# Optimization experiments

Measured on AMD Instinct MI355X. Metric: run time of the kernel, lower is better.

Reference implementation:

```python
import jax, jax.numpy as jnp
import numpy as np

N, E, KS, DIM = 6890, 41340, 5, 2
K = KS * KS  # 25 spline kernel buckets


def spline_conv(x, edge_index, pseudo, weight, root, bias):
    """Degree-1 open B-spline conv (SplineGCN), mean aggregation + root + bias.
    x: [N, Fin], weight: [K, Fin, Fout], root: [Fin, Fout], bias: [Fout]."""
    row, col = edge_index[0], edge_index[1]  # target, source
    pos = pseudo * (KS - 1)                   # [E, 2] in [0, KS-1]
    i0 = jnp.clip(jnp.floor(pos), 0, KS - 2).astype(jnp.int32)  # [E, 2]
    frac = pos - i0                           # [E, 2]
    # 4 nonzero basis products per edge (2 per dim)
    off = jnp.array([[0, 0], [1, 0], [0, 1], [1, 1]], dtype=jnp.int32)  # [4, 2]
    b_dim = jnp.stack([1.0 - frac, frac], axis=-1)  # [E, 2, 2] (dim, which-knot)
    w = b_dim[:, 0, off[:, 0]] * b_dim[:, 1, off[:, 1]]       # [E, 4]
    idx = (i0[:, None, 0] + off[None, :, 0]) + KS * (i0[:, None, 1] + off[None, :, 1])  # [E, 4]
    # transform all nodes by all K kernels once: [N, K, Fout]
    xw = jnp.einsum('ni,kio->nko', x, weight)
    g = xw[col[:, None], idx]                 # [E, 4, Fout] gather
    msg = jnp.einsum('es,eso->eo', w, g)      # [E, Fout]
    agg = jax.ops.segment_sum(msg, row, num_segments=N)
    deg = jax.ops.segment_sum(jnp.ones((E,), x.dtype), row, num_segments=N)
    agg = agg / jnp.maximum(deg, 1.0)[:, None]
    return agg + x @ root + bias


def setup_inputs() -> dict:
    key = jax.random.key(0)
    ks = jax.random.split(key, 20)
    def gl(k, shape):  # glorot-ish
        fan = shape[-2] if len(shape) > 1 else shape[-1]
        return jax.random.normal(k, shape, jnp.float32) / np.sqrt(fan)
    inp = {
        'x': jax.random.normal(ks[0], (N, 544), jnp.float32),
        'edge_index': jax.random.randint(ks[1], (2, E), 0, N),
        'pseudo': jax.random.uniform(ks[2], (E, DIM), jnp.float32),
        'W_lin': gl(ks[3], (544, 16)), 'b_lin': jnp.zeros((16,), jnp.float32),
        'w1': gl(ks[4], (K, 16, 32)),  'r1': gl(ks[5], (16, 32)),  'bi1': jnp.zeros((32,), jnp.float32),
        'w2': gl(ks[6], (K, 32, 64)),  'r2': gl(ks[7], (32, 64)),  'bi2': jnp.zeros((64,), jnp.float32),
        'w3': gl(ks[8], (K, 64, 128)), 'r3': gl(ks[9], (64, 128)), 'bi3': jnp.zeros((128,), jnp.float32),
        'W1': gl(ks[10], (128, 256)), 'b1': jnp.zeros((256,), jnp.float32),
        'W2': gl(ks[11], (256, 6890)), 'b2': jnp.zeros((6890,), jnp.float32),
    }
    return inp


def reference(x, edge_index, pseudo, W_lin, b_lin, w1, r1, bi1, w2, r2, bi2, w3, r3, bi3, W1, b1, W2, b2):
    h = jax.nn.elu(x @ W_lin + b_lin)
    h = jax.nn.elu(spline_conv(h, edge_index, pseudo, w1, r1, bi1))
    h = jax.nn.elu(spline_conv(h, edge_index, pseudo, w2, r2, bi2))
    h = jax.nn.elu(spline_conv(h, edge_index, pseudo, w3, r3, bi3))
    h = jax.nn.elu(h @ W1 + b1)
    # dropout is identity in eval mode
    logits = h @ W2 + b2
    return jax.nn.log_softmax(logits, axis=-1)
```

## Files before the change

kernel.cpp:

```cpp
#include <hip/hip_runtime.h>
#include <hip/hip_bf16.h>

#define NND 6890
#define NED 41340

typedef __bf16 bf16x8 __attribute__((ext_vector_type(8)));
typedef float f32x4 __attribute__((ext_vector_type(4)));
typedef unsigned short u16x4 __attribute__((ext_vector_type(4)));

__device__ inline unsigned short f32_bf16(float f) {
  unsigned int u = __float_as_uint(f);
  unsigned int r = (u + 0x7FFFu + ((u >> 16) & 1u)) >> 16;
  return (unsigned short)r;
}
__device__ inline void split2(float v, unsigned short& hi, unsigned short& lo) {
  unsigned short h = f32_bf16(v);
  float hf = __uint_as_float((unsigned int)h << 16);
  hi = h;
  lo = f32_bf16(v - hf);
}
__device__ inline float elu_f(float v) { return v > 0.f ? v : (expf(v) - 1.f); }

__device__ __forceinline__ void gload_lds16(const void* g, void* l) {
  __builtin_amdgcn_global_load_lds((const __attribute__((address_space(1))) void*)g,
                                   (__attribute__((address_space(3))) void*)l, 16, 0, 0);
}

__global__ void zero_int_kernel(int* p, int n) {
  int i = blockIdx.x * blockDim.x + threadIdx.x;
  if (i < n) p[i] = 0;
}

__global__ void edge_prep_kernel(const int* __restrict__ erow, const float* __restrict__ pseudo,
                                 float* __restrict__ ew, int* __restrict__ ek,
                                 int* __restrict__ deg, int E) {
  int e = blockIdx.x * blockDim.x + threadIdx.x;
  if (e >= E) return;
  float p0 = pseudo[2 * e + 0] * 4.0f;
  float p1 = pseudo[2 * e + 1] * 4.0f;
  int i0 = (int)floorf(p0); i0 = i0 < 0 ? 0 : (i0 > 3 ? 3 : i0);
  int i1 = (int)floorf(p1); i1 = i1 < 0 ? 0 : (i1 > 3 ? 3 : i1);
  float f0 = p0 - (float)i0, f1 = p1 - (float)i1;
  ew[4 * e + 0] = (1.f - f0) * (1.f - f1);
  ew[4 * e + 1] = f0 * (1.f - f1);
  ew[4 * e + 2] = (1.f - f0) * f1;
  ew[4 * e + 3] = f0 * f1;
  int b = i0 + 5 * i1;
  ek[4 * e + 0] = b; ek[4 * e + 1] = b + 1; ek[4 * e + 2] = b + 5; ek[4 * e + 3] = b + 6;
  atomicAdd(&deg[erow[e]], 1);
}

__global__ void scan_kernel(const int* __restrict__ deg, int* __restrict__ rowptr,
                            int* __restrict__ cursor, float* __restrict__ deginv, int n) {
  __shared__ int part[1024];
  int t = threadIdx.x;
  int CH = (n + 1023) >> 10;
  int base = t * CH;
  int s = 0;
  for (int j = 0; j < CH; ++j) { int i = base + j; if (i < n) s += deg[i]; }
  part[t] = s;
  __syncthreads();
  for (int off = 1; off < 1024; off <<= 1) {
    int v = (t >= off) ? part[t - off] : 0;
    __syncthreads();
    part[t] += v;
    __syncthreads();
  }
  int run = (t == 0) ? 0 : part[t - 1];
  for (int j = 0; j < CH; ++j) {
    int i = base + j;
    if (i < n) {
      rowptr[i] = run; cursor[i] = run;
      int d = deg[i];
      deginv[i] = 1.0f / fmaxf((float)d, 1.0f);
      run += d;
    }
  }
  if (t == 1023) rowptr[n] = part[1023];
}

__global__ void csr_fill_kernel(const int* __restrict__ erow, int* __restrict__ cursor,
                                int* __restrict__ csr, int E) {
  int e = blockIdx.x * blockDim.x + threadIdx.x;
  if (e >= E) return;
  int slot = atomicAdd(&cursor[erow[e]], 1);
  csr[slot] = e;
}

__global__ void split_kernel(const float* __restrict__ src, unsigned short* __restrict__ oh,
                             unsigned short* __restrict__ ol, int n4) {
  int i = blockIdx.x * 256 + threadIdx.x;
  if (i >= n4) return;
  f32x4 v = *(const f32x4*)(src + 4 * i);
  u16x4 h, l;
#pragma unroll
  for (int j = 0; j < 4; ++j) {
    unsigned short hh, ll;
    split2(v[j], hh, ll);
    h[j] = hh; l[j] = ll;
  }
  *(u16x4*)(oh + 4 * i) = h;
  *(u16x4*)(ol + 4 * i) = l;
}

__global__ void b_build_kernel(const float* __restrict__ x, const int* __restrict__ ecol,
                               const float* __restrict__ ew4, const int* __restrict__ ek4,
                               const int* __restrict__ rowptr, const int* __restrict__ csr,
                               const float* __restrict__ deginv,
                               unsigned short* __restrict__ Bh, unsigned short* __restrict__ Bl,
                               int Fin) {
  extern __shared__ float lds[];
  int r = blockIdx.x;
  int T = blockDim.x;
  int tid = threadIdx.x;
  int nb = 25 * Fin;
  int j = tid / Fin;
  int i = tid - j * Fin;
  float* plane = lds + j * nb;
  for (int t = tid; t < 4 * nb; t += T) lds[t] = 0.f;
  __syncthreads();
  int p0 = rowptr[r], p1 = rowptr[r + 1];
  for (int p = p0 + j; p < p1; p += 4) {
    int e = csr[p];
    int c = ecol[e];
    float xv = x[(size_t)c * Fin + i];
    f32x4 wv = *(const f32x4*)(ew4 + 4 * e);
    int4 kv = *(const int4*)(ek4 + 4 * e);
    plane[kv.x * Fin + i] += wv[0] * xv;
    plane[kv.y * Fin + i] += wv[1] * xv;
    plane[kv.z * Fin + i] += wv[2] * xv;
    plane[kv.w * Fin + i] += wv[3] * xv;
  }
  __syncthreads();
  float dinv = deginv[r];
  int tot = nb + Fin;
  for (int t = tid; t < tot; t += T) {
    float v;
    if (t < nb)
      v = (lds[t] + lds[nb + t] + lds[2 * nb + t] + lds[3 * nb + t]) * dinv;
    else
      v = x[(size_t)r * Fin + (t - nb)];
    unsigned short h, l;
    split2(v, h, l);
    Bh[(size_t)r * tot + t] = h;
    Bl[(size_t)r * tot + t] = l;
  }
}

__global__ void weights_prep_kernel(const float* __restrict__ W_lin, const float* __restrict__ w1,
                                    const float* __restrict__ r1, const float* __restrict__ w2,
                                    const float* __restrict__ r2, const float* __restrict__ w3,
                                    const float* __restrict__ r3, const float* __restrict__ W1,
                                    unsigned short* __restrict__ Th, unsigned short* __restrict__ Tl) {
  const int tstart[9] = {0, 17, 30, 31, 81, 83, 283, 291, 323};
  const int jK[8]    = {544, 400, 16, 800, 32, 1600, 64, 128};
  const int jF[8]    = {16, 32, 32, 64, 64, 128, 128, 256};
  const int jldt[8]  = {544, 416, 416, 832, 832, 1664, 1664, 128};
  const int jkoff[8] = {0, 0, 400, 0, 800, 0, 1600, 0};
  const int jdst[8]  = {0, 8704, 8704, 22016, 22016, 75264, 75264, 288256};
  int b = blockIdx.x;
  int job = 0;
  while (job < 7 && b >= tstart[job + 1]) ++job;
  int t = b - tstart[job];
  int fxc = (jF[job] + 31) >> 5;
  int kt = t / fxc, ft = t % fxc;
  const float* src;
  switch (job) {
    case 0: src = W_lin; break;
    case 1: src = w1; break;
    case 2: src = r1; break;
    case 3: src = w2; break;
    case 4: src = r2; break;
    case 5: src = w3; break;
    case 6: src = r3; break;
    default: src = W1; break;
  }
  int K = jK[job], F = jF[job], ldt = jldt[job], koff = jkoff[job];
  unsigned short* th = Th + jdst[job];
  unsigned short* tl = Tl + jdst[job];
  int k0 = kt * 32, c0 = ft * 32;
  __shared__ float tbuf[32][33];
  int tx = threadIdx.x & 31, ty = threadIdx.x >> 5;
  for (int j = ty; j < 32; j += 8) {
    int gk = k0 + j, gc = c0 + tx;
    tbuf[j][tx] = (gk < K && gc < F) ? src[(size_t)gk * F + gc] : 0.f;
  }
  __syncthreads();
  for (int j = ty; j < 32; j += 8) {
    int gc = c0 + j, gk = k0 + tx;
    if (gc < F && gk < K) {
      unsigned short h, lo2;
      split2(tbuf[tx][j], h, lo2);
      th[(size_t)gc * ldt + koff + gk] = h;
      tl[(size_t)gc * ldt + koff + gk] = lo2;
    }
  }
}

template <int BN>
__global__ __launch_bounds__(256) void gemm_x3_partial_kernel(
    const unsigned short* __restrict__ Ah, const unsigned short* __restrict__ Al,
    const unsigned short* __restrict__ Wh, const unsigned short* __restrict__ Wl,
    float* __restrict__ P, int M, int Kd, int F, int KS) {
  constexpr int AE = 64 * 32;
  constexpr int WE = BN * 32;
  __shared__ __align__(16) unsigned short lds[2][2 * AE + 2 * WE];
  int tid = threadIdx.x;
  int wave = tid >> 6, lane = tid & 63;
  int g = lane >> 4, r = lane & 15;
  int row0 = blockIdx.y * 64;
  int col0 = blockIdx.x * BN;
  int z = blockIdx.z;
  int nt = Kd >> 5;
  int ta = z * nt / KS, tb = (z + 1) * nt / KS;

  auto STAGE = [&](int buf, int kb) {
    {
      int rr = tid >> 2, pos = tid & 3;
      int c = (pos - rr) & 3;
      int gra = row0 + rr; if (gra >= M) gra = M - 1;
      size_t so = (size_t)gra * Kd + kb + c * 8;
      gload_lds16(Ah + so, &lds[buf][wave * 512]);
      gload_lds16(Al + so, &lds[buf][AE + wave * 512]);
    }
#pragma unroll
    for (int it = 0; it < (4 * BN + 255) / 256; ++it) {
      int idx = it * 256 + tid;
      if (idx < 4 * BN) {
        int rr = idx >> 2, pos = idx & 3;
        int c = (pos - rr) & 3;
        size_t so = (size_t)(col0 + rr) * Kd + kb + c * 8;
        gload_lds16(Wh + so, &lds[buf][2 * AE + (it * 256 + wave * 64) * 8]);
        gload_lds16(Wl + so, &lds[buf][2 * AE + WE + (it * 256 + wave * 64) * 8]);
      }
    }
  };

  constexpr int NF = BN / 16;
  f32x4 acc[NF];
#pragma unroll
  for (int n = 0; n < NF; ++n)
#pragma unroll
    for (int q = 0; q < 4; ++q) acc[n][q] = 0.f;

  int n = tb - ta;
  int rA = wave * 16 + r;
  int aoff = rA * 32 + ((g + rA) & 3) * 8;

  STAGE(0, ta * 32);
  __syncthreads();
  for (int tt = 0; tt < n; ++tt) {
    int buf = tt & 1;
    if (tt + 1 < n) STAGE(buf ^ 1, (ta + tt + 1) * 32);
    bf16x8 fah = *(const bf16x8*)&lds[buf][aoff];
    bf16x8 fal = *(const bf16x8*)&lds[buf][AE + aoff];
#pragma unroll
    for (int nn = 0; nn < NF; ++nn) {
      int rW = nn * 16 + r;
      int woff = rW * 32 + ((g + rW) & 3) * 8;
      bf16x8 fbh = *(const bf16x8*)&lds[buf][2 * AE + woff];
      bf16x8 fbl = *(const bf16x8*)&lds[buf][2 * AE + WE + woff];
      acc[nn] = __builtin_amdgcn_mfma_f32_16x16x32_bf16(fah, fbh, acc[nn], 0, 0, 0);
      acc[nn] = __builtin_amdgcn_mfma_f32_16x16x32_bf16(fal, fbh, acc[nn], 0, 0, 0);
      acc[nn] = __builtin_amdgcn_mfma_f32_16x16x32_bf16(fah, fbl, acc[nn], 0, 0, 0);
    }
    __syncthreads();
  }
#pragma unroll
  for (int nn = 0; nn < NF; ++nn) {
    int gc = col0 + nn * 16 + r;
#pragma unroll
    for (int q = 0; q < 4; ++q) {
      int gr = row0 + wave * 16 + g * 4 + q;
      if (gr < M) P[((size_t)z * M + gr) * F + gc] = acc[nn][q];
    }
  }
}

__global__ __launch_bounds__(256) void combine_elu_kernel(
    const float* __restrict__ P, const float* __restrict__ bias,
    float* __restrict__ outF, unsigned short* __restrict__ outB,
    unsigned short* __restrict__ outH, unsigned short* __restrict__ outL,
    int M, int F, int KS) {
  int i4 = blockIdx.x * 256 + threadIdx.x;
  int fv = F >> 2;
  int total = M * fv;
  if (i4 >= total) return;
  int gr = i4 / fv, c4 = (i4 - gr * fv) * 4;
  f32x4 s = {0.f, 0.f, 0.f, 0.f};
  for (int z = 0; z < KS; ++z)
    s += *(const f32x4*)(P + ((size_t)z * M + gr) * F + c4);
  f32x4 bv = *(const f32x4*)(bias + c4);
#pragma unroll
  for (int j = 0; j < 4; ++j) s[j] = elu_f(s[j] + bv[j]);
  if (outH) {
    u16x4 h, l;
#pragma unroll
    for (int j = 0; j < 4; ++j) {
      unsigned short hh, ll;
      split2(s[j], hh, ll);
      h[j] = hh; l[j] = ll;
    }
    *(u16x4*)(outH + (size_t)gr * F + c4) = h;
    *(u16x4*)(outL + (size_t)gr * F + c4) = l;
  } else if (outB) {
    u16x4 o;
#pragma unroll
    for (int j = 0; j < 4; ++j) o[j] = f32_bf16(s[j]);
    *(u16x4*)(outB + (size_t)gr * F + c4) = o;
  } else {
    *(f32x4*)(outF + (size_t)gr * F + c4) = s;
  }
}

__global__ void w2_cast_transpose_kernel(const float* __restrict__ W2,
                                         unsigned short* __restrict__ Wt, int K, int N) {
  __shared__ float t[32][33];
  int c0 = blockIdx.x * 32, k0 = blockIdx.y * 32;
  int tx = threadIdx.x, ty = threadIdx.y;
  for (int j = ty; j < 32; j += 8) {
    int gk = k0 + j, gc = c0 + tx;
    t[j][tx] = (gk < K && gc < N) ? W2[(size_t)gk * N + gc] : 0.f;
  }
  __syncthreads();
  for (int j = ty; j < 32; j += 8) {
    int gc = c0 + j, gk = k0 + tx;
    if (gc < N && gk < K) Wt[(size_t)gc * K + gk] = f32_bf16(t[tx][j]);
  }
}

template <int MODE>
__global__ __launch_bounds__(256) void gemm_final_kernel(
    const unsigned short* __restrict__ A, const unsigned short* __restrict__ Bt,
    const float* __restrict__ bias, const float* __restrict__ lse,
    float* __restrict__ outp, int M, int N) {
  __shared__ __align__(16) unsigned short lds[2][2][8192];
  int tid = threadIdx.x;
  int w = tid >> 6, l = tid & 63;
  int row0 = blockIdx.y * 128, col0 = blockIdx.x * 128;

  auto STAGE = [&](int buf, int kb) {
#pragma unroll
    for (int it = 0; it < 4; ++it) {
      int idx = it * 256 + tid;
      int rr = idx >> 3, pos = idx & 7;
      int c = (pos - rr) & 7;
      int gra = row0 + rr; if (gra >= M) gra = M - 1;
      int grb = col0 + rr; if (grb >= N) grb = N - 1;
      gload_lds16(A + (size_t)gra * 256 + kb + c * 8, &lds[buf][0][(it * 256 + w * 64) * 8]);
      gload_lds16(Bt + (size_t)grb * 256 + kb + c * 8, &lds[buf][1][(it * 256 + w * 64) * 8]);
    }
  };

  int wm = w >> 1, wn = w & 1;
  int g = l >> 4, r = l & 15;

  f32x4 acc[4][4];
#pragma unroll
  for (int mi = 0; mi < 4; ++mi)
#pragma unroll
    for (int ni = 0; ni < 4; ++ni)
#pragma unroll
      for (int q = 0; q < 4; ++q) acc[mi][ni][q] = 0.f;

  STAGE(0, 0);
  __syncthreads();
#pragma unroll
  for (int ks = 0; ks < 4; ++ks) {
    int buf = ks & 1;
    if (ks < 3) STAGE(buf ^ 1, (ks + 1) * 64);
#pragma unroll
    for (int sub = 0; sub < 2; ++sub) {
      bf16x8 fa[4], fb[4];
#pragma unroll
      for (int mi = 0; mi < 4; ++mi) {
        int rA = wm * 64 + mi * 16 + r;
        fa[mi] = *(const bf16x8*)&lds[buf][0][rA * 64 + ((g + 4 * sub + rA) & 7) * 8];
      }
#pragma unroll
      for (int ni = 0; ni < 4; ++ni) {
        int rB = wn * 64 + ni * 16 + r;
        fb[ni] = *(const bf16x8*)&lds[buf][1][rB * 64 + ((g + 4 * sub + rB) & 7) * 8];
      }
#pragma unroll
      for (int mi = 0; mi < 4; ++mi)
#pragma unroll
        for (int ni = 0; ni < 4; ++ni)
          acc[mi][ni] = __builtin_amdgcn_mfma_f32_16x16x32_bf16(fb[ni], fa[mi], acc[mi][ni], 0, 0, 0);
    }
    __syncthreads();
  }

  if (MODE == 0) {
    float bb[4][4];
#pragma unroll
    for (int ni = 0; ni < 4; ++ni) {
      int gc0 = col0 + wn * 64 + ni * 16 + g * 4;
#pragma unroll
      for (int q = 0; q < 4; ++q)
        bb[ni][q] = (gc0 + q < N) ? bias[gc0 + q] : 0.f;
    }
#pragma unroll
    for (int mi = 0; mi < 4; ++mi) {
      int gr = row0 + wm * 64 + mi * 16 + r;
      float vv[4][4];
      float mloc = -3e38f;
#pragma unroll
      for (int ni = 0; ni < 4; ++ni) {
        int gc0 = col0 + wn * 64 + ni * 16 + g * 4;
#pragma unroll
        for (int q = 0; q < 4; ++q) {
          float v = (gc0 + q < N) ? (acc[mi][ni][q] + bb[ni][q]) : -3e38f;
          vv[ni][q] = v;
          mloc = fmaxf(mloc, v);
        }
      }
      float sloc = 0.f;
#pragma unroll
      for (int ni = 0; ni < 4; ++ni) {
        int gc0 = col0 + wn * 64 + ni * 16 + g * 4;
#pragma unroll
        for (int q = 0; q < 4; ++q)
          if (gc0 + q < N) sloc += __expf(vv[ni][q] - mloc);
      }
#pragma unroll
      for (int off = 16; off < 64; off <<= 1) {
        float mo = __shfl_xor(mloc, off);
        float so = __shfl_xor(sloc, off);
        float mn = fmaxf(mloc, mo);
        sloc = sloc * __expf(mloc - mn) + so * __expf(mo - mn);
        mloc = mn;
      }
      if (g == 0 && gr < M) {
        int hb = blockIdx.x * 2 + wn;
        *(float2*)(outp + 2 * ((size_t)hb * M + gr)) = make_float2(mloc, sloc);
      }
    }
  } else {
    float* fsc = (float*)&lds[0][0][0];
    float* wbase = fsc + w * 4096;
#pragma unroll
    for (int mi = 0; mi < 4; ++mi) {
      int rr = mi * 16 + r;
#pragma unroll
      for (int ni = 0; ni < 4; ++ni) {
        int u = (ni * 4 + g + rr) & 15;
        *(f32x4*)(wbase + rr * 64 + u * 4) = acc[mi][ni];
      }
    }
    __syncthreads();
#pragma unroll
    for (int t = 0; t < 16; ++t) {
      int unit = t * 256 + tid;
      int rowi = unit >> 5, ch = unit & 31;
      int gr = row0 + rowi;
      if (gr >= M) continue;
      int reg = ((rowi >> 6) << 1) + (ch >> 4);
      int rr = rowi & 63;
      int u = ((ch & 15) + rr) & 15;
      f32x4 v = *(const f32x4*)(fsc + reg * 4096 + rr * 64 + u * 4);
      float L = lse[gr];
      int gc0 = col0 + ch * 4;
      if (gc0 + 4 <= N) {
        f32x4 bv = *(const f32x4*)(bias + gc0);
#pragma unroll
        for (int q = 0; q < 4; ++q) v[q] = v[q] + bv[q] - L;
        *(f32x4*)(outp + (size_t)gr * N + gc0) = v;
      } else {
#pragma unroll
        for (int q = 0; q < 4; ++q)
          if (gc0 + q < N) outp[(size_t)gr * N + gc0 + q] = v[q] + bias[gc0 + q] - L;
      }
    }
  }
}

__global__ __launch_bounds__(256) void lse_kernel(const float* __restrict__ stats,
                                                  float* __restrict__ lse, int M, int NH) {
  int row = blockIdx.x * 256 + threadIdx.x;
  if (row >= M) return;
  float m = -3e38f, s = 0.f;
  for (int hb = 0; hb < NH; ++hb) {
    float2 v = *(const float2*)(stats + 2 * ((size_t)hb * M + row));
    float mn = fmaxf(m, v.x);
    s = s * __expf(m - mn) + v.y * __expf(v.x - mn);
    m = mn;
  }
  lse[row] = m + logf(s);
}

extern "C" void kernel_launch(void* const* d_in, const int* in_sizes, int n_in,
                              void* d_out, int out_size, void* d_ws, size_t ws_size,
                              hipStream_t stream) {
  const int N = NND, E = NED;
  const float* x      = (const float*)d_in[0];
  const int*   ei     = (const int*)d_in[1];
  const float* pseudo = (const float*)d_in[2];
  const float* W_lin  = (const float*)d_in[3];
  const float* b_lin  = (const float*)d_in[4];
  const float* w1  = (const float*)d_in[5];
  const float* r1  = (const float*)d_in[6];
  const float* bi1 = (const float*)d_in[7];
  const float* w2  = (const float*)d_in[8];
  const float* r2  = (const float*)d_in[9];
  const float* bi2 = (const float*)d_in[10];
  const float* w3  = (const float*)d_in[11];
  const float* r3  = (const float*)d_in[12];
  const float* bi3 = (const float*)d_in[13];
  const float* W1  = (const float*)d_in[14];
  const float* b1  = (const float*)d_in[15];
  const float* W2  = (const float*)d_in[16];
  const float* b2  = (const float*)d_in[17];
  const int* erow = ei;
  const int* ecol = ei + E;

  char* scratch = (char*)d_out;
  size_t off = 0;
  auto alloc = [&](size_t bytes) -> void* {
    void* p = scratch + off;
    off = (off + bytes + 255) & ~(size_t)255;
    return p;
  };
  unsigned short* Bh = (unsigned short*)alloc((size_t)N * 1664 * 2);
  unsigned short* Bl = (unsigned short*)alloc((size_t)N * 1664 * 2);
  float* h0     = (float*)alloc((size_t)N * 16 * 4);
  float* h1     = (float*)alloc((size_t)N * 32 * 4);
  float* h2     = (float*)alloc((size_t)N * 64 * 4);
  unsigned short* h3h = (unsigned short*)alloc((size_t)N * 128 * 2);
  unsigned short* h3l = (unsigned short*)alloc((size_t)N * 128 * 2);
  unsigned short* xh  = (unsigned short*)alloc((size_t)N * 544 * 2);
  unsigned short* xl  = (unsigned short*)alloc((size_t)N * 544 * 2);
  unsigned short* Wth = (unsigned short*)alloc((size_t)321024 * 2);
  unsigned short* Wtl = (unsigned short*)alloc((size_t)321024 * 2);
  float* Pbuf   = (float*)alloc((size_t)4 * N * 128 * 4);
  float* stats  = (float*)alloc((size_t)108 * N * 2 * 4);
  float* ew     = (float*)alloc((size_t)E * 4 * 4);
  int*   ek     = (int*)alloc((size_t)E * 4 * 4);
  int*   deg    = (int*)alloc((size_t)N * 4);
  float* deginv = (float*)alloc((size_t)N * 4);
  int*   rowptr = (int*)alloc((size_t)(N + 1) * 4);
  int*   cursor = (int*)alloc((size_t)N * 4);
  int*   csr    = (int*)alloc((size_t)E * 4);

  unsigned short* h4b = (unsigned short*)d_ws;
  unsigned short* W2t = (unsigned short*)((char*)d_ws + (size_t)N * 256 * 2);
  float* lse = (float*)((char*)d_ws + (size_t)N * 256 * 4);

  zero_int_kernel<<<(N + 255) / 256, 256, 0, stream>>>(deg, N);
  edge_prep_kernel<<<(E + 255) / 256, 256, 0, stream>>>(erow, pseudo, ew, ek, deg, E);
  scan_kernel<<<1, 1024, 0, stream>>>(deg, rowptr, cursor, deginv, N);
  csr_fill_kernel<<<(E + 255) / 256, 256, 0, stream>>>(erow, cursor, csr, E);

  weights_prep_kernel<<<323, 256, 0, stream>>>(W_lin, w1, r1, w2, r2, w3, r3, W1, Wth, Wtl);
  split_kernel<<<(N * 136 + 255) / 256, 256, 0, stream>>>(x, xh, xl, N * 136);

  auto cgrid = [](int M_, int F_) { return dim3((M_ * (F_ / 4) + 255) / 256); };

  gemm_x3_partial_kernel<16><<<dim3(1, 108, 4), 256, 0, stream>>>(xh, xl, Wth + 0, Wtl + 0, Pbuf, N, 544, 16, 4);
  combine_elu_kernel<<<cgrid(N, 16), 256, 0, stream>>>(Pbuf, b_lin, h0, nullptr, nullptr, nullptr, N, 16, 4);

  b_build_kernel<<<N, 64, 4 * 25 * 16 * 4, stream>>>(h0, ecol, ew, ek, rowptr, csr, deginv, Bh, Bl, 16);
  gemm_x3_partial_kernel<32><<<dim3(1, 108, 4), 256, 0, stream>>>(Bh, Bl, Wth + 8704, Wtl + 8704, Pbuf, N, 416, 32, 4);
  combine_elu_kernel<<<cgrid(N, 32), 256, 0, stream>>>(Pbuf, bi1, h1, nullptr, nullptr, nullptr, N, 32, 4);

  b_build_kernel<<<N, 128, 4 * 25 * 32 * 4, stream>>>(h1, ecol, ew, ek, rowptr, csr, deginv, Bh, Bl, 32);
  gemm_x3_partial_kernel<64><<<dim3(1, 108, 4), 256, 0, stream>>>(Bh, Bl, Wth + 22016, Wtl + 22016, Pbuf, N, 832, 64, 4);
  combine_elu_kernel<<<cgrid(N, 64), 256, 0, stream>>>(Pbuf, bi2, h2, nullptr, nullptr, nullptr, N, 64, 4);

  b_build_kernel<<<N, 256, 4 * 25 * 64 * 4, stream>>>(h2, ecol, ew, ek, rowptr, csr, deginv, Bh, Bl, 64);
  gemm_x3_partial_kernel<128><<<dim3(1, 108, 4), 256, 0, stream>>>(Bh, Bl, Wth + 75264, Wtl + 75264, Pbuf, N, 1664, 128, 4);
  combine_elu_kernel<<<cgrid(N, 128), 256, 0, stream>>>(Pbuf, bi3, nullptr, nullptr, h3h, h3l, N, 128, 4);

  gemm_x3_partial_kernel<128><<<dim3(2, 108, 2), 256, 0, stream>>>(h3h, h3l, Wth + 288256, Wtl + 288256, Pbuf, N, 128, 256, 2);
  combine_elu_kernel<<<cgrid(N, 256), 256, 0, stream>>>(Pbuf, b1, nullptr, h4b, nullptr, nullptr, N, 256, 2);

  w2_cast_transpose_kernel<<<dim3(216, 8), dim3(32, 8), 0, stream>>>(W2, W2t, 256, N);

  gemm_final_kernel<0><<<dim3(54, 54), 256, 0, stream>>>(h4b, W2t, b2, nullptr, stats, N, N);

  lse_kernel<<<(N + 255) / 256, 256, 0, stream>>>(stats, lse, N, 108);

  gemm_final_kernel<1><<<dim3(54, 54), 256, 0, stream>>>(h4b, W2t, b2, lse, (float*)d_out, N, N);

  (void)in_sizes; (void)n_in; (void)out_size; (void)ws_size;
}
```

Measured before the change: 315.5 us.

## Merge prep kernels into one launch and halve final GEMM LDS tile

Folds the weight split/transpose, x split and W2 cast-transpose into a single prep_all_kernel launch, and replaces the zeroing kernel with hipMemsetAsync, to cut launch count and serialization. Separately, the final logits GEMM now stages 32-wide K slices instead of 64, halving its LDS footprint. Its MODE 1 epilogue is reworked into two 32-row passes through a smaller LDS buffer. The smaller LDS tile is meant to raise occupancy, at the cost of twice as many K steps and barriers.

```diff
diff --git a/kernel.cpp b/kernel.cpp
--- a/kernel.cpp
+++ b/kernel.cpp
@@ -24,11 +24,6 @@
 __device__ __forceinline__ void gload_lds16(const void* g, void* l) {
   __builtin_amdgcn_global_load_lds((const __attribute__((address_space(1))) void*)g,
                                    (__attribute__((address_space(3))) void*)l, 16, 0, 0);
-}
-
-__global__ void zero_int_kernel(int* p, int n) {
-  int i = blockIdx.x * blockDim.x + threadIdx.x;
-  if (i < n) p[i] = 0;
 }
 
 __global__ void edge_prep_kernel(const int* __restrict__ erow, const float* __restrict__ pseudo,
@@ -87,20 +82,88 @@
   csr[slot] = e;
 }
 
-__global__ void split_kernel(const float* __restrict__ src, unsigned short* __restrict__ oh,
-                             unsigned short* __restrict__ ol, int n4) {
-  int i = blockIdx.x * 256 + threadIdx.x;
-  if (i >= n4) return;
-  f32x4 v = *(const f32x4*)(src + 4 * i);
-  u16x4 h, l;
-#pragma unroll
-  for (int j = 0; j < 4; ++j) {
-    unsigned short hh, ll;
-    split2(v[j], hh, ll);
-    h[j] = hh; l[j] = ll;
-  }
-  *(u16x4*)(oh + 4 * i) = h;
-  *(u16x4*)(ol + 4 * i) = l;
+__global__ void prep_all_kernel(const float* __restrict__ W_lin, const float* __restrict__ w1,
+                                const float* __restrict__ r1, const float* __restrict__ w2,
+                                const float* __restrict__ r2, const float* __restrict__ w3,
+                                const float* __restrict__ r3, const float* __restrict__ W1,
+                                const float* __restrict__ x, const float* __restrict__ W2,
+                                unsigned short* __restrict__ Th, unsigned short* __restrict__ Tl,
+                                unsigned short* __restrict__ xh, unsigned short* __restrict__ xl,
+                                unsigned short* __restrict__ W2t) {
+  int b = blockIdx.x;
+  int tid = threadIdx.x;
+  if (b < 323) {
+    const int tstart[9] = {0, 17, 30, 31, 81, 83, 283, 291, 323};
+    const int jK[8]    = {544, 400, 16, 800, 32, 1600, 64, 128};
+    const int jF[8]    = {16, 32, 32, 64, 64, 128, 128, 256};
+    const int jldt[8]  = {544, 416, 416, 832, 832, 1664, 1664, 128};
+    const int jkoff[8] = {0, 0, 400, 0, 800, 0, 1600, 0};
+    const int jdst[8]  = {0, 8704, 8704, 22016, 22016, 75264, 75264, 288256};
+    int job = 0;
+    while (job < 7 && b >= tstart[job + 1]) ++job;
+    int t = b - tstart[job];
+    int fxc = (jF[job] + 31) >> 5;
+    int kt = t / fxc, ft = t % fxc;
+    const float* src;
+    switch (job) {
+      case 0: src = W_lin; break;
+      case 1: src = w1; break;
+      case 2: src = r1; break;
+      case 3: src = w2; break;
+      case 4: src = r2; break;
+      case 5: src = w3; break;
+      case 6: src = r3; break;
+      default: src = W1; break;
+    }
+    int K = jK[job], F = jF[job], ldt = jldt[job], koff = jkoff[job];
+    unsigned short* th = Th + jdst[job];
+    unsigned short* tl = Tl + jdst[job];
+    int k0 = kt * 32, c0 = ft * 32;
+    __shared__ float tbuf[32][33];
+    int tx = tid & 31, ty = tid >> 5;
+    for (int j = ty; j < 32; j += 8) {
+      int gk = k0 + j, gc = c0 + tx;
+      tbuf[j][tx] = (gk < K && gc < F) ? src[(size_t)gk * F + gc] : 0.f;
+    }
+    __syncthreads();
+    for (int j = ty; j < 32; j += 8) {
+      int gc = c0 + j, gk = k0 + tx;
+      if (gc < F && gk < K) {
+        unsigned short h, lo2;
+        split2(tbuf[tx][j], h, lo2);
+        th[(size_t)gc * ldt + koff + gk] = h;
+        tl[(size_t)gc * ldt + koff + gk] = lo2;
+      }
+    }
+  } else if (b < 3984) {
+    int i = (b - 323) * 256 + tid;
+    if (i < NND * 136) {
+      f32x4 v = *(const f32x4*)(x + 4 * (size_t)i);
+      u16x4 h, l;
+#pragma unroll
+      for (int j = 0; j < 4; ++j) {
+        unsigned short hh, ll;
+        split2(v[j], hh, ll);
+        h[j] = hh; l[j] = ll;
+      }
+      *(u16x4*)(xh + 4 * (size_t)i) = h;
+      *(u16x4*)(xl + 4 * (size_t)i) = l;
+    }
+  } else {
+    int t = b - 3984;
+    int c0 = (t % 216) * 32, k0 = (t / 216) * 32;
+    __shared__ float tb2[32][33];
+    int tx = tid & 31, ty = tid >> 5;
+    for (int j = ty; j < 32; j += 8) {
+      int gk = k0 + j, gc = c0 + tx;
+      tb2[j][tx] = (gk < 256 && gc < NND) ? W2[(size_t)gk * NND + gc] : 0.f;
+    }
+    __syncthreads();
+    for (int j = ty; j < 32; j += 8) {
+      int gc = c0 + j, gk = k0 + tx;
+      if (gc < NND && gk < 256) W2t[(size_t)gc * 256 + gk] = f32_bf16(tb2[tx][j]);
+    }
+  }
 }
 
 __global__ void b_build_kernel(const float* __restrict__ x, const int* __restrict__ ecol,
@@ -147,56 +210,6 @@
   }
 }
 
-__global__ void weights_prep_kernel(const float* __restrict__ W_lin, const float* __restrict__ w1,
-                                    const float* __restrict__ r1, const float* __restrict__ w2,
-                                    const float* __restrict__ r2, const float* __restrict__ w3,
-                                    const float* __restrict__ r3, const float* __restrict__ W1,
-                                    unsigned short* __restrict__ Th, unsigned short* __restrict__ Tl) {
-  const int tstart[9] = {0, 17, 30, 31, 81, 83, 283, 291, 323};
-  const int jK[8]    = {544, 400, 16, 800, 32, 1600, 64, 128};
-  const int jF[8]    = {16, 32, 32, 64, 64, 128, 128, 256};
-  const int jldt[8]  = {544, 416, 416, 832, 832, 1664, 1664, 128};
-  const int jkoff[8] = {0, 0, 400, 0, 800, 0, 1600, 0};
-  const int jdst[8]  = {0, 8704, 8704, 22016, 22016, 75264, 75264, 288256};
-  int b = blockIdx.x;
-  int job = 0;
-  while (job < 7 && b >= tstart[job + 1]) ++job;
-  int t = b - tstart[job];
-  int fxc = (jF[job] + 31) >> 5;
-  int kt = t / fxc, ft = t % fxc;
-  const float* src;
-  switch (job) {
-    case 0: src = W_lin; break;
-    case 1: src = w1; break;
-    case 2: src = r1; break;
-    case 3: src = w2; break;
-    case 4: src = r2; break;
-    case 5: src = w3; break;
-    case 6: src = r3; break;
-    default: src = W1; break;
-  }
-  int K = jK[job], F = jF[job], ldt = jldt[job], koff = jkoff[job];
-  unsigned short* th = Th + jdst[job];
-  unsigned short* tl = Tl + jdst[job];
-  int k0 = kt * 32, c0 = ft * 32;
-  __shared__ float tbuf[32][33];
-  int tx = threadIdx.x & 31, ty = threadIdx.x >> 5;
-  for (int j = ty; j < 32; j += 8) {
-    int gk = k0 + j, gc = c0 + tx;
-    tbuf[j][tx] = (gk < K && gc < F) ? src[(size_t)gk * F + gc] : 0.f;
-  }
-  __syncthreads();
-  for (int j = ty; j < 32; j += 8) {
-    int gc = c0 + j, gk = k0 + tx;
-    if (gc < F && gk < K) {
-      unsigned short h, lo2;
-      split2(tbuf[tx][j], h, lo2);
-      th[(size_t)gc * ldt + koff + gk] = h;
-      tl[(size_t)gc * ldt + koff + gk] = lo2;
-    }
-  }
-}
-
 template <int BN>
 __global__ __launch_bounds__(256) void gemm_x3_partial_kernel(
     const unsigned short* __restrict__ Ah, const unsigned short* __restrict__ Al,
@@ -313,38 +326,22 @@
   }
 }
 
-__global__ void w2_cast_transpose_kernel(const float* __restrict__ W2,
-                                         unsigned short* __restrict__ Wt, int K, int N) {
-  __shared__ float t[32][33];
-  int c0 = blockIdx.x * 32, k0 = blockIdx.y * 32;
-  int tx = threadIdx.x, ty = threadIdx.y;
-  for (int j = ty; j < 32; j += 8) {
-    int gk = k0 + j, gc = c0 + tx;
-    t[j][tx] = (gk < K && gc < N) ? W2[(size_t)gk * N + gc] : 0.f;
-  }
-  __syncthreads();
-  for (int j = ty; j < 32; j += 8) {
-    int gc = c0 + j, gk = k0 + tx;
-    if (gc < N && gk < K) Wt[(size_t)gc * K + gk] = f32_bf16(t[tx][j]);
-  }
-}
-
 template <int MODE>
 __global__ __launch_bounds__(256) void gemm_final_kernel(
     const unsigned short* __restrict__ A, const unsigned short* __restrict__ Bt,
     const float* __restrict__ bias, const float* __restrict__ lse,
     float* __restrict__ outp, int M, int N) {
-  __shared__ __align__(16) unsigned short lds[2][2][8192];
+  __shared__ __align__(16) unsigned short lds[2][2][4096];
   int tid = threadIdx.x;
   int w = tid >> 6, l = tid & 63;
   int row0 = blockIdx.y * 128, col0 = blockIdx.x * 128;
 
   auto STAGE = [&](int buf, int kb) {
 #pragma unroll
-    for (int it = 0; it < 4; ++it) {
+    for (int it = 0; it < 2; ++it) {
       int idx = it * 256 + tid;
-      int rr = idx >> 3, pos = idx & 7;
-      int c = (pos - rr) & 7;
+      int rr = idx >> 2, pos = idx & 3;
+      int c = (pos - rr) & 3;
       int gra = row0 + rr; if (gra >= M) gra = M - 1;
       int grb = col0 + rr; if (grb >= N) grb = N - 1;
       gload_lds16(A + (size_t)gra * 256 + kb + c * 8, &lds[buf][0][(it * 256 + w * 64) * 8]);
@@ -366,28 +363,25 @@
   STAGE(0, 0);
   __syncthreads();
 #pragma unroll
-  for (int ks = 0; ks < 4; ++ks) {
+  for (int ks = 0; ks < 8; ++ks) {
     int buf = ks & 1;
-    if (ks < 3) STAGE(buf ^ 1, (ks + 1) * 64);
-#pragma unroll
-    for (int sub = 0; sub < 2; ++sub) {
-      bf16x8 fa[4], fb[4];
-#pragma unroll
-      for (int mi = 0; mi < 4; ++mi) {
-        int rA = wm * 64 + mi * 16 + r;
-        fa[mi] = *(const bf16x8*)&lds[buf][0][rA * 64 + ((g + 4 * sub + rA) & 7) * 8];
-      }
-#pragma unroll
-      for (int ni = 0; ni < 4; ++ni) {
-        int rB = wn * 64 + ni * 16 + r;
-        fb[ni] = *(const bf16x8*)&lds[buf][1][rB * 64 + ((g + 4 * sub + rB) & 7) * 8];
-      }
-#pragma unroll
-      for (int mi = 0; mi < 4; ++mi)
-#pragma unroll
-        for (int ni = 0; ni < 4; ++ni)
-          acc[mi][ni] = __builtin_amdgcn_mfma_f32_16x16x32_bf16(fb[ni], fa[mi], acc[mi][ni], 0, 0, 0);
-    }
+    if (ks < 7) STAGE(buf ^ 1, (ks + 1) * 32);
+    bf16x8 fa[4], fb[4];
+#pragma unroll
+    for (int mi = 0; mi < 4; ++mi) {
+      int rA = wm * 64 + mi * 16 + r;
+      fa[mi] = *(const bf16x8*)&lds[buf][0][rA * 32 + ((g + rA) & 3) * 8];
+    }
+#pragma unroll
+    for (int ni = 0; ni < 4; ++ni) {
+      int rB = wn * 64 + ni * 16 + r;
+      fb[ni] = *(const bf16x8*)&lds[buf][1][rB * 32 + ((g + rB) & 3) * 8];
+    }
+#pragma unroll
+    for (int mi = 0; mi < 4; ++mi)
+#pragma unroll
+      for (int ni = 0; ni < 4; ++ni)
+        acc[mi][ni] = __builtin_amdgcn_mfma_f32_16x16x32_bf16(fb[ni], fa[mi], acc[mi][ni], 0, 0, 0);
     __syncthreads();
   }
 
@@ -437,39 +431,42 @@
       }
     }
   } else {
-    float* fsc = (float*)&lds[0][0][0];
-    float* wbase = fsc + w * 4096;
-#pragma unroll
-    for (int mi = 0; mi < 4; ++mi) {
-      int rr = mi * 16 + r;
-#pragma unroll
-      for (int ni = 0; ni < 4; ++ni) {
-        int u = (ni * 4 + g + rr) & 15;
-        *(f32x4*)(wbase + rr * 64 + u * 4) = acc[mi][ni];
-      }
-    }
-    __syncthreads();
-#pragma unroll
-    for (int t = 0; t < 16; ++t) {
-      int unit = t * 256 + tid;
-      int rowi = unit >> 5, ch = unit & 31;
-      int gr = row0 + rowi;
-      if (gr >= M) continue;
-      int reg = ((rowi >> 6) << 1) + (ch >> 4);
-      int rr = rowi & 63;
-      int u = ((ch & 15) + rr) & 15;
-      f32x4 v = *(const f32x4*)(fsc + reg * 4096 + rr * 64 + u * 4);
-      float L = lse[gr];
-      int gc0 = col0 + ch * 4;
-      if (gc0 + 4 <= N) {
-        f32x4 bv = *(const f32x4*)(bias + gc0);
-#pragma unroll
-        for (int q = 0; q < 4; ++q) v[q] = v[q] + bv[q] - L;
-        *(f32x4*)(outp + (size_t)gr * N + gc0) = v;
-      } else {
-#pragma unroll
-        for (int q = 0; q < 4; ++q)
-          if (gc0 + q < N) outp[(size_t)gr * N + gc0 + q] = v[q] + bias[gc0 + q] - L;
+    float* LBUF = (float*)&lds[0][0][0];
+#pragma unroll
+    for (int p = 0; p < 2; ++p) {
+      __syncthreads();
+#pragma unroll
+      for (int mh = 0; mh < 2; ++mh) {
+        int mi = 2 * p + mh;
+        int lr = wm * 32 + mh * 16 + r;
+#pragma unroll
+        for (int ni = 0; ni < 4; ++ni) {
+          int ch = wn * 16 + ni * 4 + g;
+          int u = (ch + lr) & 31;
+          *(f32x4*)(LBUF + lr * 128 + u * 4) = acc[mi][ni];
+        }
+      }
+      __syncthreads();
+#pragma unroll
+      for (int t = 0; t < 8; ++t) {
+        int unit = t * 256 + tid;
+        int lr = unit >> 5, ch = unit & 31;
+        int gr = row0 + (lr >> 5) * 64 + p * 32 + ((lr >> 4) & 1) * 16 + (lr & 15);
+        if (gr >= M) continue;
+        int u = (ch + lr) & 31;
+        f32x4 v = *(const f32x4*)(LBUF + lr * 128 + u * 4);
+        float L = lse[gr];
+        int gc0 = col0 + ch * 4;
+        if (gc0 + 4 <= N) {
+          f32x4 bv = *(const f32x4*)(bias + gc0);
+#pragma unroll
+          for (int q = 0; q < 4; ++q) v[q] = v[q] + bv[q] - L;
+          *(f32x4*)(outp + (size_t)gr * N + gc0) = v;
+        } else {
+#pragma unroll
+          for (int q = 0; q < 4; ++q)
+            if (gc0 + q < N) outp[(size_t)gr * N + gc0 + q] = v[q] + bias[gc0 + q] - L;
+        }
       }
     }
   }
@@ -546,13 +543,13 @@
   unsigned short* W2t = (unsigned short*)((char*)d_ws + (size_t)N * 256 * 2);
   float* lse = (float*)((char*)d_ws + (size_t)N * 256 * 4);
 
-  zero_int_kernel<<<(N + 255) / 256, 256, 0, stream>>>(deg, N);
+  hipMemsetAsync(deg, 0, (size_t)N * 4, stream);
   edge_prep_kernel<<<(E + 255) / 256, 256, 0, stream>>>(erow, pseudo, ew, ek, deg, E);
   scan_kernel<<<1, 1024, 0, stream>>>(deg, rowptr, cursor, deginv, N);
   csr_fill_kernel<<<(E + 255) / 256, 256, 0, stream>>>(erow, cursor, csr, E);
 
-  weights_prep_kernel<<<323, 256, 0, stream>>>(W_lin, w1, r1, w2, r2, w3, r3, W1, Wth, Wtl);
-  split_kernel<<<(N * 136 + 255) / 256, 256, 0, stream>>>(x, xh, xl, N * 136);
+  prep_all_kernel<<<5712, 256, 0, stream>>>(W_lin, w1, r1, w2, r2, w3, r3, W1, x, W2,
+                                            Wth, Wtl, xh, xl, W2t);
 
   auto cgrid = [](int M_, int F_) { return dim3((M_ * (F_ / 4) + 255) / 256); };
 
@@ -574,8 +571,6 @@
   gemm_x3_partial_kernel<128><<<dim3(2, 108, 2), 256, 0, stream>>>(h3h, h3l, Wth + 288256, Wtl + 288256, Pbuf, N, 128, 256, 2);
   combine_elu_kernel<<<cgrid(N, 256), 256, 0, stream>>>(Pbuf, b1, nullptr, h4b, nullptr, nullptr, N, 256, 2);
 
-  w2_cast_transpose_kernel<<<dim3(216, 8), dim3(32, 8), 0, stream>>>(W2, W2t, 256, N);
-
   gemm_final_kernel<0><<<dim3(54, 54), 256, 0, stream>>>(h4b, W2t, b2, nullptr, stats, N, N);
 
   lse_kernel<<<(N + 255) / 256, 256, 0, stream>>>(stats, lse, N, 108);
```

New measurement: 306.3 us. 2.9% less time.
